# Kernel tuning notes

Hardware: AMD Instinct MI355X
Metric: run time of the kernel (lower is better)

Reference implementation:

```python
import math
import jax, jax.numpy as jnp
import numpy as np

B, T, D, H = 4, 2048, 1024, 16
DH = D // H


def setup_inputs() -> dict:
    key = jax.random.key(0)
    ks = jax.random.split(key, 12)
    s = 1.0 / math.sqrt(D)
    return {
        "query": jax.random.normal(ks[0], (B, T, D), jnp.float32),
        "key": jax.random.normal(ks[1], (B, T, D), jnp.float32),
        "value": jax.random.normal(ks[2], (B, T, D), jnp.float32),
        "mask": jax.random.randint(ks[3], (1, 1, T, T), 0, 2).astype(jnp.bool_),
        "Wq": jax.random.normal(ks[4], (D, D), jnp.float32) * s,
        "bq": jnp.zeros((D,), jnp.float32),
        "Wk": jax.random.normal(ks[5], (D, D), jnp.float32) * s,
        "bk": jnp.zeros((D,), jnp.float32),
        "Wv": jax.random.normal(ks[6], (D, D), jnp.float32) * s,
        "bv": jnp.zeros((D,), jnp.float32),
        "Wo": jax.random.normal(ks[7], (D, D), jnp.float32) * s,
        "bo": jnp.zeros((D,), jnp.float32),
    }


def _heads(x):
    # [B,T,D] -> [B,H,T,DH]
    b, t, _ = x.shape
    return x.reshape(b, t, H, DH).transpose(0, 2, 1, 3)


def reference(query, key, value, mask, Wq, bq, Wk, bk, Wv, bv, Wo, bo):
    q = _heads(query @ Wq.T + bq)
    k = _heads(key @ Wk.T + bk)
    v = _heads(value @ Wv.T + bv)
    # NOTE: original scales by 1/sqrt(embed_dim), not head_dim
    logits = jnp.einsum('bhqd,bhkd->bhqk', q, k) / math.sqrt(D)
    logits = jnp.where(mask, -jnp.inf, logits)
    scores = jax.nn.softmax(logits, axis=-1)
    o = jnp.einsum('bhqk,bhkd->bhqd', scores, v)  # [B,H,T,DH]
    o = o.transpose(0, 2, 1, 3).reshape(query.shape[0], -1, D)
    return o @ Wo.T + bo
```

## Files before the change

kernel.cpp:

```cpp
#include <hip/hip_runtime.h>
#include <hip/hip_bf16.h>

#define D_MODEL 1024
#define SEQ     2048
#define BATCH   4
#define NH      16
#define DHEAD   64

typedef __attribute__((ext_vector_type(8))) short bhalf8;
typedef __attribute__((ext_vector_type(4))) float floatx4;
typedef __attribute__((ext_vector_type(16))) float floatx16;
typedef __attribute__((ext_vector_type(4))) unsigned int uintx4;

__device__ __forceinline__ void gload16(const void* g, void* l) {
  __builtin_amdgcn_global_load_lds(
      (const __attribute__((address_space(1))) unsigned int*)g,
      (__attribute__((address_space(3))) unsigned int*)l, 16, 0, 0);
}

__device__ __forceinline__ unsigned short f2bf(float x) {
  __hip_bfloat16 h = __float2bfloat16(x);
  return __builtin_bit_cast(unsigned short, h);
}

__global__ void cvt_bf16_kernel(const float* __restrict__ in,
                                unsigned short* __restrict__ out, int n4) {
  int i = blockIdx.x * blockDim.x + threadIdx.x;
  if (i >= n4) return;
  float4 v = ((const float4*)in)[i];
  ushort4 o;
  o.x = f2bf(v.x); o.y = f2bf(v.y); o.z = f2bf(v.z); o.w = f2bf(v.w);
  ((ushort4*)out)[i] = o;
}

__global__ void detect_mask_kernel(const unsigned int* __restrict__ m,
                                   unsigned int* __restrict__ flag) {
  __shared__ unsigned int not_int, not_flt;
  if (threadIdx.x == 0) { not_int = 0u; not_flt = 0u; }
  __syncthreads();
  unsigned int ni = 0u, nf = 0u;
  for (int j = 0; j < 4; ++j) {
    unsigned int w = m[threadIdx.x * 4 + j];
    if (w > 1u) ni = 1u;
    if (w != 0u && w != 0x3f800000u) nf = 1u;
  }
  if (ni) atomicOr(&not_int, 1u);
  if (nf) atomicOr(&not_flt, 1u);
  __syncthreads();
  if (threadIdx.x == 0) {
    unsigned int f = 1u;
    if (!not_int) f = 0u;
    else if (!not_flt) f = 2u;
    *flag = f;
  }
}

__global__ void pack_mask_kernel(const void* __restrict__ mraw,
                                 const unsigned int* __restrict__ flag,
                                 unsigned long long* __restrict__ bits) {
  int t = blockIdx.x * blockDim.x + threadIdx.x;
  unsigned int f = *flag;
  int v;
  if (f == 1u) v = (((const unsigned char*)mraw)[t] != 0);
  else         v = (((const unsigned int*)mraw)[t] != 0u);
  unsigned long long b = __ballot(v);
  if ((threadIdx.x & 63) == 0) bits[t >> 6] = b;
}

template <int MODE>
__global__ __launch_bounds__(256, 2)
void gemm_nt_kernel(const unsigned short* __restrict__ A,
                    const unsigned short* __restrict__ B,
                    const float* __restrict__ bias, void* __restrict__ Cout,
                    int M, int N, int K, float scale) {
  __shared__ unsigned short As[2][128][64];
  __shared__ unsigned short Bs[2][128][64];
  const int tid = threadIdx.x;
  const int wid = tid >> 6, lane = tid & 63;
  const int g = lane >> 4, c = lane & 15;
  const int wr = wid >> 1, wc = wid & 1;

  const int L = blockIdx.x;
  const int xcd = L & 7;
  const int i5 = L >> 3;
  const int u = i5 & 7, v5 = i5 >> 3;
  int bx, by;
  if ((N >> 7) == 8) { bx = u; by = xcd + 8 * v5; }
  else               { bx = xcd + 8 * u; by = v5; }
  const int m0 = by * 128, n0 = bx * 128;

  const floatx4 zero4 = {0.f, 0.f, 0.f, 0.f};
  floatx4 acc[4][4];
#pragma unroll
  for (int i = 0; i < 4; ++i)
#pragma unroll
    for (int j = 0; j < 4; ++j) acc[i][j] = zero4;

  const int r_ = tid >> 3;
  const int sb = ((tid & 7) * 16) ^ (((tid >> 3) & 7) << 4);
  const char* Asrc = (const char*)(A + (size_t)(m0 + r_) * K) + sb;
  const char* Bsrc = (const char*)(B + (size_t)(n0 + r_) * K) + sb;
  const size_t ROWP = (size_t)32 * K * 2;

  auto stage = [&](int kt, int buf) {
    const size_t ko = (size_t)kt * 128;
#pragma unroll
    for (int p = 0; p < 4; ++p) {
      gload16(Asrc + ko + p * ROWP, (char*)&As[buf][0][0] + p * 4096 + tid * 16);
      gload16(Bsrc + ko + p * ROWP, (char*)&Bs[buf][0][0] + p * 4096 + tid * 16);
    }
  };

  const int nkt = K >> 6;
  stage(0, 0);
  __syncthreads();
  int cur = 0;
  for (int kt = 0; kt < nkt; ++kt) {
    if (kt + 1 < nkt) stage(kt + 1, cur ^ 1);
    const char* abase = (const char*)&As[cur][0][0];
    const char* bbase = (const char*)&Bs[cur][0][0];
    bhalf8 a[2][4], b[2][4];
#pragma unroll
    for (int kk = 0; kk < 2; ++kk) {
#pragma unroll
      for (int i = 0; i < 4; ++i) {
        const int row = wr * 64 + i * 16 + c;
        a[kk][i] = *(const bhalf8*)(abase + row * 128 +
                                    ((kk * 64 + g * 16) ^ ((row & 7) << 4)));
      }
#pragma unroll
      for (int j = 0; j < 4; ++j) {
        const int row = wc * 64 + j * 16 + c;
        b[kk][j] = *(const bhalf8*)(bbase + row * 128 +
                                    ((kk * 64 + g * 16) ^ ((row & 7) << 4)));
      }
    }
#pragma unroll
    for (int kk = 0; kk < 2; ++kk)
#pragma unroll
      for (int i = 0; i < 4; ++i)
#pragma unroll
        for (int j = 0; j < 4; ++j)
          acc[i][j] = __builtin_amdgcn_mfma_f32_16x16x32_bf16(a[kk][i], b[kk][j], acc[i][j], 0, 0, 0);
    __syncthreads();
    cur ^= 1;
  }

  float bn[4] = {0.f, 0.f, 0.f, 0.f};
  if (MODE != 1) {
#pragma unroll
    for (int j = 0; j < 4; ++j) bn[j] = bias[n0 + wc * 64 + j * 16 + c];
  }
#pragma unroll
  for (int i = 0; i < 4; ++i) {
    float bm[4] = {0.f, 0.f, 0.f, 0.f};
    if (MODE == 1) {
#pragma unroll
      for (int r = 0; r < 4; ++r) bm[r] = bias[m0 + wr * 64 + i * 16 + 4 * g + r];
    }
#pragma unroll
    for (int j = 0; j < 4; ++j) {
#pragma unroll
      for (int r = 0; r < 4; ++r) {
        const int m = m0 + wr * 64 + i * 16 + 4 * g + r;
        const int n = n0 + wc * 64 + j * 16 + c;
        const float v = (acc[i][j][r] + ((MODE == 1) ? bm[r] : bn[j])) * scale;
        if (MODE == 2) ((float*)Cout)[(size_t)m * N + n] = v;
        else ((unsigned short*)Cout)[(size_t)m * N + n] = f2bf(v);
      }
    }
  }
}

__global__ __launch_bounds__(256, 3)
void attn_kernel(const unsigned short* __restrict__ Q,
                 const unsigned short* __restrict__ Kmat,
                 const unsigned short* __restrict__ Vt,
                 const unsigned long long* __restrict__ mbits,
                 unsigned short* __restrict__ O) {
  __shared__ unsigned short Ks[2][64][64];
  __shared__ unsigned short Vs[2][64][64];

  const int tid = threadIdx.x;
  const int wid = tid >> 6, lane = tid & 63;
  const int ql = lane & 31;
  const int hi = lane >> 5;

  const int L = blockIdx.x;
  const int xcd = L & 7;
  const int s = L >> 3;
  const int bh = (s & 7) * 8 + xcd;
  const int qt = s >> 3;
  const int b = bh >> 4, h = bh & 15;
  const int q0 = qt * 128 + wid * 32;

  const unsigned short* Qb = Q + (size_t)(b * SEQ + q0) * D_MODEL + h * DHEAD;
  const unsigned short* Kb = Kmat + (size_t)(b * SEQ) * D_MODEL + h * DHEAD;
  const unsigned short* Vb = Vt + (size_t)(h * DHEAD) * (BATCH * SEQ) + (size_t)b * SEQ;

  bhalf8 qf[4];
#pragma unroll
  for (int ks = 0; ks < 4; ++ks)
    qf[ks] = *(const bhalf8*)(Qb + (size_t)ql * D_MODEL + ks * 16 + hi * 8);

  const floatx16 z16 = {0,0,0,0,0,0,0,0,0,0,0,0,0,0,0,0};
  floatx16 ot[2];
  ot[0] = z16; ot[1] = z16;
  floatx16 lt = z16;

  const short ONEB = (short)0x3F80;
  const bhalf8 ones8 = {ONEB, ONEB, ONEB, ONEB, ONEB, ONEB, ONEB, ONEB};

  int koff[4];
#pragma unroll
  for (int ks = 0; ks < 4; ++ks)
    koff[ks] = ql * 128 + ((ks * 32 + hi * 16) ^ ((ql & 7) << 4));

  const int sr = tid >> 3;
  const int sbz = ((tid & 7) * 16) ^ ((sr & 7) << 4);
  const char* Ksrc = (const char*)(Kb + (size_t)sr * D_MODEL) + sbz;
  const char* Vsrc = (const char*)(Vb + (size_t)sr * (BATCH * SEQ)) + sbz;
  const size_t KR32 = (size_t)32 * D_MODEL * 2;
  const size_t VR32 = (size_t)32 * (BATCH * SEQ) * 2;
  const size_t KSTEP = (size_t)64 * D_MODEL * 2;
  const size_t VSTEP = 128;

  const int NT = SEQ / 64;
  gload16(Ksrc,        (char*)&Ks[0][0][0] + tid * 16);
  gload16(Ksrc + KR32, (char*)&Ks[0][0][0] + 4096 + tid * 16);
  gload16(Vsrc,        (char*)&Vs[0][0][0] + tid * 16);
  gload16(Vsrc + VR32, (char*)&Vs[0][0][0] + 4096 + tid * 16);
  __syncthreads();
  const char* kp = Ksrc + KSTEP;
  const char* vp = Vsrc + VSTEP;
  const unsigned long long* mp = mbits + (size_t)(q0 + ql) * (SEQ / 64);
  int cur = 0;

  for (int kt = 0; kt < NT; ++kt) {
    if (kt + 1 < NT) {
      gload16(kp,        (char*)&Ks[cur ^ 1][0][0] + tid * 16);
      gload16(kp + KR32, (char*)&Ks[cur ^ 1][0][0] + 4096 + tid * 16);
      gload16(vp,        (char*)&Vs[cur ^ 1][0][0] + tid * 16);
      gload16(vp + VR32, (char*)&Vs[cur ^ 1][0][0] + 4096 + tid * 16);
      kp += KSTEP;
      vp += VSTEP;
    }
    const unsigned long long mws = mp[kt] >> (4 * hi);
    const unsigned int mlo = (unsigned int)mws;
    const unsigned int mhi32 = (unsigned int)(mws >> 32);

    const char* kbase = (const char*)&Ks[cur][0][0];
    const char* vbase = (const char*)&Vs[cur][0][0];

    floatx16 st[2];
    st[0] = z16; st[1] = z16;
    __builtin_amdgcn_s_setprio(1);
#pragma unroll
    for (int ks = 0; ks < 4; ++ks) {
#pragma unroll
      for (int blk = 0; blk < 2; ++blk) {
        const bhalf8 kf = *(const bhalf8*)(kbase + koff[ks] + blk * 4096);
        st[blk] = __builtin_amdgcn_mfma_f32_32x32x16_bf16(kf, qf[ks], st[blk], 0, 0, 0);
      }
    }
    __builtin_amdgcn_s_setprio(0);

    unsigned int w[2][8];
#pragma unroll
    for (int blk = 0; blk < 2; ++blk) {
      const unsigned int word = blk ? mhi32 : mlo;
#pragma unroll
      for (int i = 0; i < 8; ++i) {
        const int r0 = 2 * i, r1 = 2 * i + 1;
        const int c0 = (r0 & 3) + 8 * (r0 >> 2);
        const int c1 = (r1 & 3) + 8 * (r1 >> 2);
        float p0 = __builtin_amdgcn_exp2f(st[blk][r0]);
        float p1 = __builtin_amdgcn_exp2f(st[blk][r1]);
        if ((word >> c0) & 1u) p0 = 0.f;
        if ((word >> c1) & 1u) p1 = 0.f;
        w[blk][i] = ((unsigned int)f2bf(p1) << 16) | (unsigned int)f2bf(p0);
      }
    }

    unsigned int x[2][8];
#pragma unroll
    for (int blk = 0; blk < 2; ++blk)
#pragma unroll
      for (int i = 0; i < 8; ++i) x[blk][i] = __shfl_xor(w[blk][i], 32);

    __builtin_amdgcn_s_setprio(1);
#pragma unroll
    for (int blk = 0; blk < 2; ++blk)
#pragma unroll
      for (int s2 = 0; s2 < 2; ++s2) {
        const int ks = blk * 2 + s2;
        const int o = s2 * 4;
        uintx4 awv;
        awv[0] = hi ? x[blk][o + 2] : w[blk][o + 0];
        awv[1] = hi ? x[blk][o + 3] : w[blk][o + 1];
        awv[2] = hi ? w[blk][o + 2] : x[blk][o + 0];
        awv[3] = hi ? w[blk][o + 3] : x[blk][o + 1];
        const bhalf8 pa = __builtin_bit_cast(bhalf8, awv);
#pragma unroll
        for (int db = 0; db < 2; ++db) {
          const bhalf8 vf = *(const bhalf8*)(vbase + koff[ks] + db * 4096);
          ot[db] = __builtin_amdgcn_mfma_f32_32x32x16_bf16(pa, vf, ot[db], 0, 0, 0);
        }
        lt = __builtin_amdgcn_mfma_f32_32x32x16_bf16(pa, ones8, lt, 0, 0, 0);
      }
    __builtin_amdgcn_s_setprio(0);

    __syncthreads();
    cur ^= 1;
  }

#pragma unroll
  for (int r = 0; r < 16; ++r) {
    const int qr = (r & 3) + 8 * (r >> 2) + 4 * hi;
    const float fi = 1.f / lt[r];
    unsigned short* orow = O + (size_t)(b * SEQ + q0 + qr) * D_MODEL + h * DHEAD + ql;
    orow[0]  = f2bf(ot[0][r] * fi);
    orow[32] = f2bf(ot[1][r] * fi);
  }
}

extern "C" void kernel_launch(void* const* d_in, const int* in_sizes, int n_in,
                              void* d_out, int out_size, void* d_ws, size_t ws_size,
                              hipStream_t stream) {
  (void)in_sizes; (void)n_in; (void)out_size;
  const float* query = (const float*)d_in[0];
  const float* key   = (const float*)d_in[1];
  const float* value = (const float*)d_in[2];
  const void*  mask  = d_in[3];
  const float* Wq = (const float*)d_in[4];
  const float* bq = (const float*)d_in[5];
  const float* Wk = (const float*)d_in[6];
  const float* bk = (const float*)d_in[7];
  const float* Wv = (const float*)d_in[8];
  const float* bv = (const float*)d_in[9];
  const float* Wo = (const float*)d_in[10];
  const float* bo = (const float*)d_in[11];

  char* ws = (char*)d_ws;
  size_t off = 0;
  auto alloc = [&](size_t bytes) {
    char* p = ws + off;
    off += (bytes + 255) & ~(size_t)255;
    return p;
  };
  unsigned short* Xb  = (unsigned short*)alloc((size_t)8192 * 1024 * 2);
  unsigned short* Wb  = (unsigned short*)alloc((size_t)1024 * 1024 * 2);
  unsigned short* Qb  = (unsigned short*)alloc((size_t)8192 * 1024 * 2);
  unsigned short* Kbf = (unsigned short*)alloc((size_t)8192 * 1024 * 2);
  unsigned short* Vtb = (unsigned short*)alloc((size_t)8192 * 1024 * 2);
  unsigned short* Ob  = (unsigned short*)alloc((size_t)8192 * 1024 * 2);
  unsigned long long* mbits = (unsigned long long*)alloc((size_t)2048 * 32 * 8);
  unsigned int* flag = (unsigned int*)alloc(256);
  if (off > ws_size) return;

  const float QSCALE = 1.4426950408889634f / 32.0f;

  detect_mask_kernel<<<1, 256, 0, stream>>>((const unsigned int*)mask, flag);
  pack_mask_kernel<<<(SEQ * SEQ) / 256, 256, 0, stream>>>(mask, flag, mbits);

  cvt_bf16_kernel<<<8192, 256, 0, stream>>>(query, Xb, 2097152);
  cvt_bf16_kernel<<<1024, 256, 0, stream>>>(Wq, Wb, 262144);
  gemm_nt_kernel<0><<<dim3(512), 256, 0, stream>>>(Xb, Wb, bq, Qb, 8192, 1024, 1024, QSCALE);
  cvt_bf16_kernel<<<8192, 256, 0, stream>>>(key, Xb, 2097152);
  cvt_bf16_kernel<<<1024, 256, 0, stream>>>(Wk, Wb, 262144);
  gemm_nt_kernel<0><<<dim3(512), 256, 0, stream>>>(Xb, Wb, bk, Kbf, 8192, 1024, 1024, 1.0f);
  cvt_bf16_kernel<<<8192, 256, 0, stream>>>(value, Xb, 2097152);
  cvt_bf16_kernel<<<1024, 256, 0, stream>>>(Wv, Wb, 262144);
  gemm_nt_kernel<1><<<dim3(512), 256, 0, stream>>>(Wb, Xb, bv, Vtb, 1024, 8192, 1024, 1.0f);
  attn_kernel<<<dim3(1024), 256, 0, stream>>>(Qb, Kbf, Vtb, mbits, Ob);
  cvt_bf16_kernel<<<1024, 256, 0, stream>>>(Wo, Wb, 262144);
  gemm_nt_kernel<2><<<dim3(512), 256, 0, stream>>>(Ob, Wb, bo, (float*)d_out, 8192, 1024, 1024, 1.0f);
}
```

Before: 251.3 us.

## Batch bf16 conversions and Q/K/V projections into single launches, branchless mask

All seven fp32-to-bf16 conversions now run in one kernel writing to separate buffers, and the three Q/K/V projection GEMMs run as one 1536-block launch. This cuts launch count and lets the three GEMMs fill the GPU together instead of running back to back. The mask bits are inverted at pack time so the attention kernel can zero masked probabilities with a bitwise AND instead of a branch-based select. It needs more workspace, and a fallback path keeps the old sequential schedule when the workspace is too small.

New measurement: 246.1 us. 2.1% less time.

```diff
diff --git a/kernel.cpp b/kernel.cpp
--- a/kernel.cpp
+++ b/kernel.cpp
@@ -21,6 +21,11 @@
 __device__ __forceinline__ unsigned short f2bf(float x) {
   __hip_bfloat16 h = __float2bfloat16(x);
   return __builtin_bit_cast(unsigned short, h);
+}
+
+__device__ __forceinline__ float andmask(float p, unsigned int w, int c) {
+  const unsigned int e = (unsigned int)(((int)(w << (31 - c))) >> 31);
+  return __builtin_bit_cast(float, __builtin_bit_cast(unsigned int, p) & e);
 }
 
 __global__ void cvt_bf16_kernel(const float* __restrict__ in,
@@ -31,6 +36,32 @@
   ushort4 o;
   o.x = f2bf(v.x); o.y = f2bf(v.y); o.z = f2bf(v.z); o.w = f2bf(v.w);
   ((ushort4*)out)[i] = o;
+}
+
+__global__ void cvt_all_kernel(const float* __restrict__ q, const float* __restrict__ k,
+                               const float* __restrict__ v, const float* __restrict__ wq,
+                               const float* __restrict__ wk, const float* __restrict__ wv,
+                               const float* __restrict__ wo,
+                               unsigned short* __restrict__ xq, unsigned short* __restrict__ xk,
+                               unsigned short* __restrict__ xv, unsigned short* __restrict__ wqb,
+                               unsigned short* __restrict__ wkb, unsigned short* __restrict__ wvb,
+                               unsigned short* __restrict__ wob) {
+  const int L = blockIdx.x;
+  const float* src;
+  unsigned short* dst;
+  int base;
+  if      (L < 8192)  { src = q;  dst = xq;  base = 0; }
+  else if (L < 16384) { src = k;  dst = xk;  base = 8192; }
+  else if (L < 24576) { src = v;  dst = xv;  base = 16384; }
+  else if (L < 25600) { src = wq; dst = wqb; base = 24576; }
+  else if (L < 26624) { src = wk; dst = wkb; base = 25600; }
+  else if (L < 27648) { src = wv; dst = wvb; base = 26624; }
+  else                { src = wo; dst = wob; base = 27648; }
+  const int i = (L - base) * 256 + threadIdx.x;
+  float4 vv = ((const float4*)src)[i];
+  ushort4 o;
+  o.x = f2bf(vv.x); o.y = f2bf(vv.y); o.z = f2bf(vv.z); o.w = f2bf(vv.w);
+  ((ushort4*)dst)[i] = o;
 }
 
 __global__ void detect_mask_kernel(const unsigned int* __restrict__ m,
@@ -63,16 +94,16 @@
   int v;
   if (f == 1u) v = (((const unsigned char*)mraw)[t] != 0);
   else         v = (((const unsigned int*)mraw)[t] != 0u);
-  unsigned long long b = __ballot(v);
+  unsigned long long b = __ballot(v == 0);
   if ((threadIdx.x & 63) == 0) bits[t >> 6] = b;
 }
 
-template <int MODE>
-__global__ __launch_bounds__(256, 2)
-void gemm_nt_kernel(const unsigned short* __restrict__ A,
-                    const unsigned short* __restrict__ B,
-                    const float* __restrict__ bias, void* __restrict__ Cout,
-                    int M, int N, int K, float scale) {
+template <int F32OUT>
+__device__ __forceinline__ void gemm_core(const unsigned short* __restrict__ A,
+                                          const unsigned short* __restrict__ B,
+                                          const float* __restrict__ bias,
+                                          void* __restrict__ Cout,
+                                          int N, float scale, int biasM, int L) {
   __shared__ unsigned short As[2][128][64];
   __shared__ unsigned short Bs[2][128][64];
   const int tid = threadIdx.x;
@@ -80,7 +111,6 @@
   const int g = lane >> 4, c = lane & 15;
   const int wr = wid >> 1, wc = wid & 1;
 
-  const int L = blockIdx.x;
   const int xcd = L & 7;
   const int i5 = L >> 3;
   const int u = i5 & 7, v5 = i5 >> 3;
@@ -98,9 +128,9 @@
 
   const int r_ = tid >> 3;
   const int sb = ((tid & 7) * 16) ^ (((tid >> 3) & 7) << 4);
-  const char* Asrc = (const char*)(A + (size_t)(m0 + r_) * K) + sb;
-  const char* Bsrc = (const char*)(B + (size_t)(n0 + r_) * K) + sb;
-  const size_t ROWP = (size_t)32 * K * 2;
+  const char* Asrc = (const char*)(A + (size_t)(m0 + r_) * 1024) + sb;
+  const char* Bsrc = (const char*)(B + (size_t)(n0 + r_) * 1024) + sb;
+  const size_t ROWP = (size_t)32 * 1024 * 2;
 
   auto stage = [&](int kt, int buf) {
     const size_t ko = (size_t)kt * 128;
@@ -111,12 +141,11 @@
     }
   };
 
-  const int nkt = K >> 6;
   stage(0, 0);
   __syncthreads();
   int cur = 0;
-  for (int kt = 0; kt < nkt; ++kt) {
-    if (kt + 1 < nkt) stage(kt + 1, cur ^ 1);
+  for (int kt = 0; kt < 16; ++kt) {
+    if (kt + 1 < 16) stage(kt + 1, cur ^ 1);
     const char* abase = (const char*)&As[cur][0][0];
     const char* bbase = (const char*)&Bs[cur][0][0];
     bhalf8 a[2][4], b[2][4];
@@ -147,14 +176,14 @@
   }
 
   float bn[4] = {0.f, 0.f, 0.f, 0.f};
-  if (MODE != 1) {
+  if (!biasM) {
 #pragma unroll
     for (int j = 0; j < 4; ++j) bn[j] = bias[n0 + wc * 64 + j * 16 + c];
   }
 #pragma unroll
   for (int i = 0; i < 4; ++i) {
     float bm[4] = {0.f, 0.f, 0.f, 0.f};
-    if (MODE == 1) {
+    if (biasM) {
 #pragma unroll
       for (int r = 0; r < 4; ++r) bm[r] = bias[m0 + wr * 64 + i * 16 + 4 * g + r];
     }
@@ -164,12 +193,42 @@
       for (int r = 0; r < 4; ++r) {
         const int m = m0 + wr * 64 + i * 16 + 4 * g + r;
         const int n = n0 + wc * 64 + j * 16 + c;
-        const float v = (acc[i][j][r] + ((MODE == 1) ? bm[r] : bn[j])) * scale;
-        if (MODE == 2) ((float*)Cout)[(size_t)m * N + n] = v;
+        const float v = (acc[i][j][r] + (biasM ? bm[r] : bn[j])) * scale;
+        if (F32OUT) ((float*)Cout)[(size_t)m * N + n] = v;
         else ((unsigned short*)Cout)[(size_t)m * N + n] = f2bf(v);
       }
     }
   }
+}
+
+__global__ __launch_bounds__(256, 2)
+void gemm_qkv_kernel(const unsigned short* __restrict__ Xq,
+                     const unsigned short* __restrict__ Xk,
+                     const unsigned short* __restrict__ Xv,
+                     const unsigned short* __restrict__ Wqb,
+                     const unsigned short* __restrict__ Wkb,
+                     const unsigned short* __restrict__ Wvb,
+                     const float* __restrict__ bq, const float* __restrict__ bk,
+                     const float* __restrict__ bv,
+                     unsigned short* __restrict__ Qb, unsigned short* __restrict__ Kb,
+                     unsigned short* __restrict__ Vtb, float qscale, int jsel) {
+  int j, L;
+  if (jsel == 3) { j = blockIdx.x >> 9; L = blockIdx.x & 511; }
+  else           { j = jsel; L = blockIdx.x; }
+  const unsigned short* A = (j == 0) ? Xq : (j == 1) ? Xk : Wvb;
+  const unsigned short* B = (j == 0) ? Wqb : (j == 1) ? Wkb : Xv;
+  const float* bias = (j == 0) ? bq : (j == 1) ? bk : bv;
+  unsigned short* C = (j == 0) ? Qb : (j == 1) ? Kb : Vtb;
+  const int N = (j == 2) ? 8192 : 1024;
+  const float scale = (j == 0) ? qscale : 1.0f;
+  gemm_core<0>(A, B, bias, C, N, scale, (j == 2) ? 1 : 0, L);
+}
+
+__global__ __launch_bounds__(256, 2)
+void gemm_out_kernel(const unsigned short* __restrict__ A,
+                     const unsigned short* __restrict__ B,
+                     const float* __restrict__ bias, float* __restrict__ C) {
+  gemm_core<1>(A, B, bias, C, 1024, 1.0f, 0, blockIdx.x);
 }
 
 __global__ __launch_bounds__(256, 3)
@@ -274,10 +333,8 @@
         const int r0 = 2 * i, r1 = 2 * i + 1;
         const int c0 = (r0 & 3) + 8 * (r0 >> 2);
         const int c1 = (r1 & 3) + 8 * (r1 >> 2);
-        float p0 = __builtin_amdgcn_exp2f(st[blk][r0]);
-        float p1 = __builtin_amdgcn_exp2f(st[blk][r1]);
-        if ((word >> c0) & 1u) p0 = 0.f;
-        if ((word >> c1) & 1u) p1 = 0.f;
+        const float p0 = andmask(__builtin_amdgcn_exp2f(st[blk][r0]), word, c0);
+        const float p1 = andmask(__builtin_amdgcn_exp2f(st[blk][r1]), word, c1);
         w[blk][i] = ((unsigned int)f2bf(p1) << 16) | (unsigned int)f2bf(p0);
       }
     }
@@ -341,6 +398,11 @@
   const float* Wo = (const float*)d_in[10];
   const float* bo = (const float*)d_in[11];
 
+  const float QSCALE = 1.4426950408889634f / 32.0f;
+  const size_t XB = (size_t)8192 * 1024 * 2;
+  const size_t WB = (size_t)1024 * 1024 * 2;
+  const size_t MB = (size_t)2048 * 32 * 8;
+
   char* ws = (char*)d_ws;
   size_t off = 0;
   auto alloc = [&](size_t bytes) {
@@ -348,31 +410,67 @@
     off += (bytes + 255) & ~(size_t)255;
     return p;
   };
-  unsigned short* Xb  = (unsigned short*)alloc((size_t)8192 * 1024 * 2);
-  unsigned short* Wb  = (unsigned short*)alloc((size_t)1024 * 1024 * 2);
-  unsigned short* Qb  = (unsigned short*)alloc((size_t)8192 * 1024 * 2);
-  unsigned short* Kbf = (unsigned short*)alloc((size_t)8192 * 1024 * 2);
-  unsigned short* Vtb = (unsigned short*)alloc((size_t)8192 * 1024 * 2);
-  unsigned short* Ob  = (unsigned short*)alloc((size_t)8192 * 1024 * 2);
-  unsigned long long* mbits = (unsigned long long*)alloc((size_t)2048 * 32 * 8);
+
+  {
+    size_t o2 = 0;
+    auto need = [&](size_t b) { o2 += (b + 255) & ~(size_t)255; };
+    need(XB); need(XB); need(XB);
+    need(WB); need(WB); need(WB); need(WB);
+    need(XB); need(XB); need(XB);
+    need(MB); need(256);
+    if (o2 <= ws_size) {
+      unsigned short* Xq  = (unsigned short*)alloc(XB);
+      unsigned short* Xk  = (unsigned short*)alloc(XB);
+      unsigned short* Xv  = (unsigned short*)alloc(XB);
+      unsigned short* Wqb = (unsigned short*)alloc(WB);
+      unsigned short* Wkb = (unsigned short*)alloc(WB);
+      unsigned short* Wvb = (unsigned short*)alloc(WB);
+      unsigned short* Wob = (unsigned short*)alloc(WB);
+      unsigned short* Qb  = (unsigned short*)alloc(XB);
+      unsigned short* Kbf = (unsigned short*)alloc(XB);
+      unsigned short* Vtb = (unsigned short*)alloc(XB);
+      unsigned long long* mbits = (unsigned long long*)alloc(MB);
+      unsigned int* flag = (unsigned int*)alloc(256);
+      unsigned short* Ob = Xq;
+
+      detect_mask_kernel<<<1, 256, 0, stream>>>((const unsigned int*)mask, flag);
+      pack_mask_kernel<<<(SEQ * SEQ) / 256, 256, 0, stream>>>(mask, flag, mbits);
+      cvt_all_kernel<<<28672, 256, 0, stream>>>(query, key, value, Wq, Wk, Wv, Wo,
+                                                Xq, Xk, Xv, Wqb, Wkb, Wvb, Wob);
+      gemm_qkv_kernel<<<1536, 256, 0, stream>>>(Xq, Xk, Xv, Wqb, Wkb, Wvb,
+                                                bq, bk, bv, Qb, Kbf, Vtb, QSCALE, 3);
+      attn_kernel<<<1024, 256, 0, stream>>>(Qb, Kbf, Vtb, mbits, Ob);
+      gemm_out_kernel<<<512, 256, 0, stream>>>(Ob, Wob, bo, (float*)d_out);
+      return;
+    }
+  }
+
+  unsigned short* Xb  = (unsigned short*)alloc(XB);
+  unsigned short* Wb  = (unsigned short*)alloc(WB);
+  unsigned short* Qb  = (unsigned short*)alloc(XB);
+  unsigned short* Kbf = (unsigned short*)alloc(XB);
+  unsigned short* Vtb = (unsigned short*)alloc(XB);
+  unsigned short* Ob  = (unsigned short*)alloc(XB);
+  unsigned long long* mbits = (unsigned long long*)alloc(MB);
   unsigned int* flag = (unsigned int*)alloc(256);
   if (off > ws_size) return;
 
-  const float QSCALE = 1.4426950408889634f / 32.0f;
-
   detect_mask_kernel<<<1, 256, 0, stream>>>((const unsigned int*)mask, flag);
   pack_mask_kernel<<<(SEQ * SEQ) / 256, 256, 0, stream>>>(mask, flag, mbits);
 
   cvt_bf16_kernel<<<8192, 256, 0, stream>>>(query, Xb, 2097152);
   cvt_bf16_kernel<<<1024, 256, 0, stream>>>(Wq, Wb, 262144);
-  gemm_nt_kernel<0><<<dim3(512), 256, 0, stream>>>(Xb, Wb, bq, Qb, 8192, 1024, 1024, QSCALE);
+  gemm_qkv_kernel<<<512, 256, 0, stream>>>(Xb, Xb, Xb, Wb, Wb, Wb, bq, bk, bv,
+                                           Qb, Kbf, Vtb, QSCALE, 0);
   cvt_bf16_kernel<<<8192, 256, 0, stream>>>(key, Xb, 2097152);
   cvt_bf16_kernel<<<1024, 256, 0, stream>>>(Wk, Wb, 262144);
-  gemm_nt_kernel<0><<<dim3(512), 256, 0, stream>>>(Xb, Wb, bk, Kbf, 8192, 1024, 1024, 1.0f);
+  gemm_qkv_kernel<<<512, 256, 0, stream>>>(Xb, Xb, Xb, Wb, Wb, Wb, bq, bk, bv,
+                                           Qb, Kbf, Vtb, QSCALE, 1);
   cvt_bf16_kernel<<<8192, 256, 0, stream>>>(value, Xb, 2097152);
   cvt_bf16_kernel<<<1024, 256, 0, stream>>>(Wv, Wb, 262144);
-  gemm_nt_kernel<1><<<dim3(512), 256, 0, stream>>>(Wb, Xb, bv, Vtb, 1024, 8192, 1024, 1.0f);
-  attn_kernel<<<dim3(1024), 256, 0, stream>>>(Qb, Kbf, Vtb, mbits, Ob);
+  gemm_qkv_kernel<<<512, 256, 0, stream>>>(Xb, Xb, Xb, Wb, Wb, Wb, bq, bk, bv,
+                                           Qb, Kbf, Vtb, QSCALE, 2);
+  attn_kernel<<<1024, 256, 0, stream>>>(Qb, Kbf, Vtb, mbits, Ob);
   cvt_bf16_kernel<<<1024, 256, 0, stream>>>(Wo, Wb, 262144);
-  gemm_nt_kernel<2><<<dim3(512), 256, 0, stream>>>(Ob, Wb, bo, (float*)d_out, 8192, 1024, 1024, 1.0f);
-}
+  gemm_out_kernel<<<512, 256, 0, stream>>>(Ob, Wb, bo, (float*)d_out);
+}
```
